# Kernel tuning notes

Hardware: AMD Instinct MI355X
Metric: run time of the kernel (lower is better)

## Reference

```python
import jax, jax.numpy as jnp
import numpy as np

D_MODEL = 1024
N_HEADS = 16
HEAD_D = D_MODEL // N_HEADS  # 64


def setup_inputs() -> dict:
    key = jax.random.key(0)
    ks = jax.random.split(key, 10)
    s = 1.0 / np.sqrt(D_MODEL)
    x = jax.random.normal(ks[0], (4, 2048, D_MODEL), dtype=jnp.float32)
    # Per-head Q/K/V linears stacked along a head axis: W [H, d_model, d], b [H, d]
    Wq = jax.random.uniform(ks[1], (N_HEADS, D_MODEL, HEAD_D), jnp.float32, -s, s)
    bq = jax.random.uniform(ks[2], (N_HEADS, HEAD_D), jnp.float32, -s, s)
    Wk = jax.random.uniform(ks[3], (N_HEADS, D_MODEL, HEAD_D), jnp.float32, -s, s)
    bk = jax.random.uniform(ks[4], (N_HEADS, HEAD_D), jnp.float32, -s, s)
    Wv = jax.random.uniform(ks[5], (N_HEADS, D_MODEL, HEAD_D), jnp.float32, -s, s)
    bv = jax.random.uniform(ks[6], (N_HEADS, HEAD_D), jnp.float32, -s, s)
    Wo = jax.random.uniform(ks[7], (D_MODEL, D_MODEL), jnp.float32, -s, s)
    bo = jax.random.uniform(ks[8], (D_MODEL,), jnp.float32, -s, s)
    return {"x": x, "Wq": Wq, "bq": bq, "Wk": Wk, "bk": bk,
            "Wv": Wv, "bv": bv, "Wo": Wo, "bo": bo}


def reference(x, Wq, bq, Wk, bk, Wv, bv, Wo, bo):
    # x: [B, S, M]; per-head projections -> [B, H, S, d]
    Q = jnp.einsum('bsm,hmd->bhsd', x, Wq) + bq[None, :, None, :]
    K = jnp.einsum('bsm,hmd->bhsd', x, Wk) + bk[None, :, None, :]
    V = jnp.einsum('bsm,hmd->bhsd', x, Wv) + bv[None, :, None, :]
    scale = 1.0 / jnp.sqrt(jnp.asarray(HEAD_D, dtype=x.dtype))
    scores = jnp.einsum('bhqd,bhkd->bhqk', Q, K) * scale  # [B, H, S, S]
    attn = jax.nn.softmax(scores, axis=-1)
    out = jnp.einsum('bhqk,bhkd->bhqd', attn, V)  # [B, H, S, d]
    B, H, S, d = out.shape
    out = out.transpose(0, 2, 1, 3).reshape(B, S, H * d)  # concat heads
    # final projection (dropout is identity in eval mode)
    return out @ Wo.T + bo
```

## Files before the change

kernel.cpp:

```cpp
#include <hip/hip_runtime.h>
#include <stdint.h>

#define DEVI __device__ __forceinline__

typedef float f32x4 __attribute__((ext_vector_type(4)));
typedef float f32x16 __attribute__((ext_vector_type(16)));
typedef float float4v __attribute__((ext_vector_type(4)));
typedef short short8 __attribute__((ext_vector_type(8)));
typedef uint16_t u16x4 __attribute__((ext_vector_type(4)));
typedef uint32_t u32x4 __attribute__((ext_vector_type(4)));
typedef int i32x2 __attribute__((ext_vector_type(2)));

static constexpr float QSCALE = 0.125f * 1.44269504088896340736f;

DEVI uint16_t f2bf(float f) {
  uint32_t u = __builtin_bit_cast(uint32_t, f);
  return (uint16_t)((u + 0x7FFFu + ((u >> 16) & 1u)) >> 16);
}

DEVI void gload_lds16(const void* g, void* lds) {
  __builtin_amdgcn_global_load_lds(
      reinterpret_cast<const uint32_t __attribute__((address_space(1)))*>(
          reinterpret_cast<uintptr_t>(g)),
      reinterpret_cast<uint32_t __attribute__((address_space(3)))*>(
          reinterpret_cast<uintptr_t>(lds)),
      16, 0, 0);
}

DEVI short8 lds_frag(const uint16_t* tile, int row, int kByte) {
  return *(const short8*)((const char*)tile + row * 128 + (kByte ^ ((row & 7) << 4)));
}

DEVI short8 frag256(const uint16_t* tile, int row, int j) {
  return *(const short8*)((const char*)tile + row * 256 + (((j ^ (row & 15)) << 4)));
}

DEVI f32x4 mfma16(short8 a, short8 b, f32x4 c) {
  return __builtin_amdgcn_mfma_f32_16x16x32_bf16(a, b, c, 0, 0, 0);
}
DEVI f32x16 mfma32(short8 a, short8 b, f32x16 c) {
  return __builtin_amdgcn_mfma_f32_32x32x16_bf16(a, b, c, 0, 0, 0);
}

DEVI uint32_t cvtpk(float lo, float hi) {
  uint32_t r;
  asm("v_cvt_pk_bf16_f32 %0, %1, %2" : "=v"(r) : "v"(lo), "v"(hi));
  return r;
}

DEVI void mk_pa(const f32x16& p0, const f32x16& p1, short8* pa) {
#pragma unroll
  for (int km = 0; km < 2; ++km) {
#pragma unroll
    for (int bb = 0; bb < 2; ++bb) {
      const f32x16& p = km ? p1 : p0;
      uint32_t X0 = cvtpk(p[8 * bb + 0], p[8 * bb + 1]);
      uint32_t Y0 = cvtpk(p[8 * bb + 4], p[8 * bb + 5]);
      uint32_t X1 = cvtpk(p[8 * bb + 2], p[8 * bb + 3]);
      uint32_t Y1 = cvtpk(p[8 * bb + 6], p[8 * bb + 7]);
      i32x2 s0 = __builtin_amdgcn_permlane32_swap((int)X0, (int)Y0, false, false);
      i32x2 s1 = __builtin_amdgcn_permlane32_swap((int)X1, (int)Y1, false, false);
      u32x4 dw = {(uint32_t)s0[0], (uint32_t)s1[0], (uint32_t)s0[1], (uint32_t)s1[1]};
      pa[km * 2 + bb] = __builtin_bit_cast(short8, dw);
    }
  }
}

DEVI float tree_sum(const f32x16& p0, const f32x16& p1) {
  float s[16];
#pragma unroll
  for (int r = 0; r < 16; ++r) s[r] = p0[r] + p1[r];
#pragma unroll
  for (int r = 0; r < 8; ++r) s[r] += s[r + 8];
#pragma unroll
  for (int r = 0; r < 4; ++r) s[r] += s[r + 4];
  return (s[0] + s[1]) + (s[2] + s[3]);
}

__global__ void k_prep(const float* __restrict__ x, const float* __restrict__ Wq,
                       const float* __restrict__ Wk, const float* __restrict__ Wv,
                       const float* __restrict__ Wo, uint16_t* __restrict__ xb,
                       uint16_t* __restrict__ Wt, uint16_t* __restrict__ Wob) {
  __shared__ float tile[64][65];
  const int bx = blockIdx.x, t = threadIdx.x;
  if (bx < 4608) {
    const float* src = (bx < 4096) ? x : Wo;
    uint16_t* dst = (bx < 4096) ? xb : Wob;
    const int i = (bx < 4096 ? bx : bx - 4096) * 256 + t;
    const float4v* p = (const float4v*)src + (size_t)i * 2;
    float4v a = p[0], b = p[1];
    alignas(16) uint16_t r[8];
    r[0] = f2bf(a[0]); r[1] = f2bf(a[1]); r[2] = f2bf(a[2]); r[3] = f2bf(a[3]);
    r[4] = f2bf(b[0]); r[5] = f2bf(b[1]); r[6] = f2bf(b[2]); r[7] = f2bf(b[3]);
    *((short8*)dst + i) = *(const short8*)r;
    return;
  }
  const int bq = bx - 4608;
  const int sect = bq >> 8, h = (bq >> 4) & 15, kc = bq & 15;
  const float* W = sect == 0 ? Wq : (sect == 1 ? Wk : Wv);
  const float scal = sect == 0 ? QSCALE : 1.0f;
  const int r = t >> 2, cbase = (t & 3) * 16;
  const float* src = W + ((size_t)(h * 1024 + kc * 64 + r)) * 64 + cbase;
#pragma unroll
  for (int j = 0; j < 4; ++j) {
    float4v v = *(const float4v*)(src + j * 4);
    tile[r][cbase + j * 4 + 0] = v[0];
    tile[r][cbase + j * 4 + 1] = v[1];
    tile[r][cbase + j * 4 + 2] = v[2];
    tile[r][cbase + j * 4 + 3] = v[3];
  }
  __syncthreads();
  const int dd = t >> 2, kp = (t & 3) * 16;
  alignas(16) uint16_t tmp[16];
#pragma unroll
  for (int j = 0; j < 16; ++j) tmp[j] = f2bf(tile[kp + j][dd] * scal);
  const int n = sect * 1024 + h * 64 + dd;
  uint16_t* dst = Wt + (size_t)n * 1024 + kc * 64 + kp;
  *(short8*)dst = *(const short8*)tmp;
  *((short8*)dst + 1) = *(const short8*)(tmp + 8);
}

template <int MODE>
__global__ __launch_bounds__(256, 2) void gemm_k1024(
    const uint16_t* __restrict__ A, const uint16_t* __restrict__ Bt, int tiles_n,
    const float* __restrict__ bias_q, const float* __restrict__ bias_k,
    const float* __restrict__ bias_v,
    uint16_t* __restrict__ Qws, uint16_t* __restrict__ Kws, uint16_t* __restrict__ Vtws,
    float* __restrict__ outf) {
  __shared__ uint16_t As[2][128 * 64];
  __shared__ uint16_t Bs[2][128 * 64];

  const int tid = threadIdx.x, lane = tid & 63, wv = tid >> 6;
  const int cpx = (MODE == 0) ? 192 : 64;
  const int bid = blockIdx.x;
  const int swz = (bid & 7) * cpx + (bid >> 3);
  const int m0 = (swz / tiles_n) * 128;
  const int n0 = (swz % tiles_n) * 128;
  const int wm = (wv >> 1) * 64, wn = (wv & 1) * 64;
  const int rin = lane >> 3;
  const int csw = ((lane & 7) ^ rin) * 16;

  const char* gA = (const char*)A;
  const char* gB = (const char*)Bt;

  f32x4 acc[4][4];
#pragma unroll
  for (int mi = 0; mi < 4; ++mi)
#pragma unroll
    for (int ni = 0; ni < 4; ++ni) acc[mi][ni] = (f32x4){0.f, 0.f, 0.f, 0.f};

  auto stage = [&](int buf, int kt) {
    const int k0b = kt * 128;
#pragma unroll
    for (int i = 0; i < 4; ++i) {
      const int rb = wv * 32 + i * 8;
      gload_lds16(gA + (size_t)(m0 + rb + rin) * 2048 + k0b + csw, &As[buf][rb * 64]);
      gload_lds16(gB + (size_t)(n0 + rb + rin) * 2048 + k0b + csw, &Bs[buf][rb * 64]);
    }
  };

  stage(0, 0);
  const int kb0 = (lane >> 4) * 16;
  for (int kt = 0; kt < 16; ++kt) {
    const int buf = kt & 1;
    __syncthreads();
    if (kt + 1 < 16) stage(buf ^ 1, kt + 1);
#pragma unroll
    for (int kk = 0; kk < 2; ++kk) {
      short8 af[4], bfr[4];
#pragma unroll
      for (int i = 0; i < 4; ++i) {
        af[i] = lds_frag(As[buf], wm + i * 16 + (lane & 15), kk * 64 + kb0);
        bfr[i] = lds_frag(Bs[buf], wn + i * 16 + (lane & 15), kk * 64 + kb0);
      }
#pragma unroll
      for (int mi = 0; mi < 4; ++mi)
#pragma unroll
        for (int ni = 0; ni < 4; ++ni) acc[mi][ni] = mfma16(af[mi], bfr[ni], acc[mi][ni]);
    }
    __syncthreads();
  }

  const int col0 = n0 + wn + (lane & 15);
  const int row0 = m0 + wm + ((lane >> 4) << 2);
  if (MODE == 1) {
#pragma unroll
    for (int ni = 0; ni < 4; ++ni) {
      const int n = col0 + ni * 16;
      const float bv = bias_q[n];
#pragma unroll
      for (int mi = 0; mi < 4; ++mi) {
        const int mrow = row0 + mi * 16;
#pragma unroll
        for (int r = 0; r < 4; ++r)
          outf[(size_t)(mrow + r) * 1024 + n] = acc[mi][ni][r] + bv;
      }
    }
  } else if (n0 >= 2048) {
    const int h = ((n0 + wn) >> 6) & 15;
    const int mbase = m0 + wm;
    const int b = mbase >> 11, sbase = mbase & 2047;
    const int bh = b * 16 + h;
    char* ep = (char*)&As[0][0] + wv * 8192;
#pragma unroll
    for (int ni = 0; ni < 4; ++ni) {
      const int dd = ni * 16 + (lane & 15);
      const float bv = bias_v[h * 64 + dd];
#pragma unroll
      for (int mi = 0; mi < 4; ++mi) {
#pragma unroll
        for (int r = 0; r < 4; ++r) {
          const int s = mi * 16 + ((lane >> 4) << 2) + r;
          *(uint16_t*)(ep + dd * 128 + ((s * 2) ^ ((dd & 7) << 4))) =
              f2bf(acc[mi][ni][r] + bv);
        }
      }
    }
#pragma unroll
    for (int it = 0; it < 8; ++it) {
      const int dd = it * 8 + (lane >> 3), c = lane & 7;
      short8 vv = *(const short8*)(ep + dd * 128 + ((c * 16) ^ ((dd & 7) << 4)));
      *(short8*)(Vtws + ((size_t)bh * 64 + dd) * 2048 + sbase + c * 8) = vv;
    }
  } else {
#pragma unroll
    for (int ni = 0; ni < 4; ++ni) {
      const int n = col0 + ni * 16;
      const int sect = n >> 10, h = (n >> 6) & 15, dd = n & 63;
      const float bv = (sect == 0) ? bias_q[h * 64 + dd] * QSCALE : bias_k[h * 64 + dd];
#pragma unroll
      for (int mi = 0; mi < 4; ++mi) {
        const int mrow = row0 + mi * 16;
        const int b = mrow >> 11, s = mrow & 2047;
        const int bh = b * 16 + h;
        uint16_t* dst = (sect == 0 ? Qws : Kws) + ((size_t)bh * 2048 + s) * 64 + dd;
#pragma unroll
        for (int r = 0; r < 4; ++r) dst[(size_t)r * 64] = f2bf(acc[mi][ni][r] + bv);
      }
    }
  }
}

__global__ __launch_bounds__(256, 2) void attn_fa(
    const uint16_t* __restrict__ Qws, const uint16_t* __restrict__ Kws,
    const uint16_t* __restrict__ Vtws, uint16_t* __restrict__ AttO) {
  __shared__ uint16_t SM[2][2][32 * 128];

  const int tid = threadIdx.x, lane = tid & 63, wq = tid >> 6;
  const int bid = blockIdx.x;
  const int bh = (bid & 7) * 8 + (bid >> 6);
  const int q0 = ((bid >> 3) & 7) * 256;
  const int hi = lane >> 5;
  const int qc = lane & 31;

  const uint16_t* Qb = Qws + (size_t)bh * (2048 * 64);
  const uint16_t* Kb = Kws + (size_t)bh * (2048 * 64);
  const uint16_t* Vb = Vtws + (size_t)bh * (64 * 2048);

  const int srow = lane >> 4;
  const int lchunk = lane & 15;

  short8 qf[2][4];
#pragma unroll
  for (int g = 0; g < 2; ++g)
#pragma unroll
    for (int c = 0; c < 4; ++c)
      qf[g][c] = *(const short8*)(Qb + (size_t)(q0 + wq * 64 + g * 32 + qc) * 64 +
                                  c * 16 + hi * 8);

  f32x16 oA0 = {}, oA1 = {}, oB0 = {}, oB1 = {};
  float lA = 0.0f, lB = 0.0f;

  auto stage = [&](int buf, int kt) {
    const int kv0 = kt * 64;
#pragma unroll
    for (int i = 0; i < 2; ++i) {
      const int rb = wq * 8 + i * 4;
      const int rt = rb + srow;
      const int j = lchunk ^ (rt & 15);
      const int jh = (j & 8) ? 32 : 0, jl = (j & 7) * 8;
      gload_lds16(Kb + (size_t)(kv0 + rt + jh) * 64 + jl,
                  (char*)&SM[buf][0][0] + rb * 256);
      gload_lds16(Vb + (size_t)(rt + jh) * 2048 + kv0 + jl,
                  (char*)&SM[buf][1][0] + rb * 256);
    }
  };

  stage(0, 0);
  for (int kt = 0; kt < 32; ++kt) {
    const int buf = kt & 1;
    __syncthreads();
    if (kt + 1 < 32) stage(buf ^ 1, kt + 1);
    const uint16_t* Kl = &SM[buf][0][0];
    const uint16_t* Vl = &SM[buf][1][0];

    f32x16 pA0 = {}, pA1 = {}, pB0 = {}, pB1 = {};
    __builtin_amdgcn_s_setprio(1);
#pragma unroll
    for (int c = 0; c < 4; ++c) {
      short8 k0 = frag256(Kl, qc, c * 2 + hi);
      short8 k1 = frag256(Kl, qc, 8 + c * 2 + hi);
      pA0 = mfma32(k0, qf[0][c], pA0);
      pA1 = mfma32(k1, qf[0][c], pA1);
      pB0 = mfma32(k0, qf[1][c], pB0);
      pB1 = mfma32(k1, qf[1][c], pB1);
    }
    __builtin_amdgcn_s_setprio(0);

    short8 paA[4], paB[4];
#pragma unroll
    for (int r = 0; r < 16; ++r) pA0[r] = __builtin_amdgcn_exp2f(pA0[r]);
#pragma unroll
    for (int r = 0; r < 16; ++r) pA1[r] = __builtin_amdgcn_exp2f(pA1[r]);
    lA += tree_sum(pA0, pA1);
    mk_pa(pA0, pA1, paA);
#pragma unroll
    for (int r = 0; r < 16; ++r) pB0[r] = __builtin_amdgcn_exp2f(pB0[r]);
#pragma unroll
    for (int r = 0; r < 16; ++r) pB1[r] = __builtin_amdgcn_exp2f(pB1[r]);
    lB += tree_sum(pB0, pB1);
    mk_pa(pB0, pB1, paB);

    __builtin_amdgcn_s_setprio(1);
#pragma unroll
    for (int ks = 0; ks < 4; ++ks) {
      short8 v0 = frag256(Vl, qc, ks * 2 + hi);
      short8 v1 = frag256(Vl, qc, 8 + ks * 2 + hi);
      oA0 = mfma32(v0, paA[ks], oA0);
      oA1 = mfma32(v1, paA[ks], oA1);
      oB0 = mfma32(v0, paB[ks], oB0);
      oB1 = mfma32(v1, paB[ks], oB1);
    }
    __builtin_amdgcn_s_setprio(0);
    __syncthreads();
  }
  lA += __shfl_xor(lA, 32, 64);
  lB += __shfl_xor(lB, 32, 64);

  const float invA = 1.0f / lA, invB = 1.0f / lB;
#pragma unroll
  for (int r = 0; r < 16; ++r) {
    oA0[r] *= invA; oA1[r] *= invA;
    oB0[r] *= invB; oB1[r] *= invB;
  }

  char* ep = (char*)&SM[0][0][0] + wq * 8192;
#pragma unroll
  for (int g = 0; g < 2; ++g)
#pragma unroll
    for (int no = 0; no < 2; ++no)
#pragma unroll
      for (int rg = 0; rg < 4; ++rg) {
        const f32x16& oo = g ? (no ? oB1 : oB0) : (no ? oA1 : oA0);
        const int row = g * 32 + qc;
        const int d0 = no * 32 + rg * 8 + hi * 4;
        u16x4 pk;
#pragma unroll
        for (int j = 0; j < 4; ++j) pk[j] = f2bf(oo[rg * 4 + j]);
        *(u16x4*)(ep + row * 128 + ((d0 * 2) ^ ((row & 7) << 4))) = pk;
      }
  const int b = bh >> 4, h = bh & 15;
#pragma unroll
  for (int it = 0; it < 8; ++it) {
    const int pos = it * 64 + lane;
    const int qq = pos >> 3, c = pos & 7;
    short8 vv = *(const short8*)(ep + qq * 128 + ((c * 16) ^ ((qq & 7) << 4)));
    *(short8*)(AttO + ((size_t)b * 2048 + q0 + wq * 64 + qq) * 1024 + h * 64 + c * 8) = vv;
  }
}


extern "C" void kernel_launch(void* const* d_in, const int* in_sizes, int n_in,
                              void* d_out, int out_size, void* d_ws, size_t ws_size,
                              hipStream_t stream) {
  (void)in_sizes; (void)n_in; (void)out_size; (void)ws_size;
  const float* x  = (const float*)d_in[0];
  const float* Wq = (const float*)d_in[1];
  const float* bq = (const float*)d_in[2];
  const float* Wk = (const float*)d_in[3];
  const float* bk = (const float*)d_in[4];
  const float* Wv = (const float*)d_in[5];
  const float* bv = (const float*)d_in[6];
  const float* Wo = (const float*)d_in[7];
  const float* bo = (const float*)d_in[8];
  float* out = (float*)d_out;

  char* ws = (char*)d_ws;
  uint16_t* Xb   = (uint16_t*)(ws);
  uint16_t* AttO = (uint16_t*)(ws);
  uint16_t* Wqkv = (uint16_t*)(ws + 16777216);
  uint16_t* Wob  = (uint16_t*)(ws + 23068672);
  uint16_t* Qws  = (uint16_t*)(ws + 25165824);
  uint16_t* Kws  = (uint16_t*)(ws + 41943040);
  uint16_t* Vt   = (uint16_t*)(ws + 58720256);

  k_prep<<<5376, 256, 0, stream>>>(x, Wq, Wk, Wv, Wo, Xb, Wqkv, Wob);
  gemm_k1024<0><<<64 * 24, 256, 0, stream>>>(Xb, Wqkv, 24, bq, bk, bv, Qws, Kws, Vt, nullptr);
  attn_fa<<<512, 256, 0, stream>>>(Qws, Kws, Vt, AttO);
  gemm_k1024<1><<<64 * 8, 256, 0, stream>>>(AttO, Wob, 8, bo, nullptr, nullptr,
                                            nullptr, nullptr, nullptr, out);
}
```

Before: 162.7 us.

## Prefetch two K-tiles ahead with explicit vmcnt waits in GEMM mainloop

The GEMM mainloop now issues global->LDS loads two stages ahead. Each iteration waits only for the older tile's loads via s_waitcnt vmcnt(8) instead of a full __syncthreads. All LDS fragments for both k-substeps are read into registers, followed by a barrier, before the buffer is refilled for tile kt+2. The MFMA block runs at raised wave priority, letting the next global loads overlap the matrix math. This costs extra fragment registers and relies on exact hand-counted outstanding-load numbers.

Measured after the change: 165.4 us. About the same (+1.6%).

```diff
diff --git a/kernel.cpp b/kernel.cpp
--- a/kernel.cpp
+++ b/kernel.cpp
@@ -160,25 +160,40 @@
   };
 
   stage(0, 0);
+  stage(1, 1);
   const int kb0 = (lane >> 4) * 16;
   for (int kt = 0; kt < 16; ++kt) {
     const int buf = kt & 1;
-    __syncthreads();
-    if (kt + 1 < 16) stage(buf ^ 1, kt + 1);
-#pragma unroll
-    for (int kk = 0; kk < 2; ++kk) {
-      short8 af[4], bfr[4];
+    if (kt < 15) asm volatile("s_waitcnt vmcnt(8)" ::: "memory");
+    else         asm volatile("s_waitcnt vmcnt(0)" ::: "memory");
+    __builtin_amdgcn_sched_barrier(0);
+    __builtin_amdgcn_s_barrier();
+    __builtin_amdgcn_sched_barrier(0);
+
+    short8 af[2][4], bfr[2][4];
+#pragma unroll
+    for (int kk = 0; kk < 2; ++kk)
 #pragma unroll
       for (int i = 0; i < 4; ++i) {
-        af[i] = lds_frag(As[buf], wm + i * 16 + (lane & 15), kk * 64 + kb0);
-        bfr[i] = lds_frag(Bs[buf], wn + i * 16 + (lane & 15), kk * 64 + kb0);
+        af[kk][i] = lds_frag(As[buf], wm + i * 16 + (lane & 15), kk * 64 + kb0);
+        bfr[kk][i] = lds_frag(Bs[buf], wn + i * 16 + (lane & 15), kk * 64 + kb0);
       }
+    asm volatile("s_waitcnt lgkmcnt(0)" ::: "memory");
+    __builtin_amdgcn_sched_barrier(0);
+    __builtin_amdgcn_s_barrier();
+    __builtin_amdgcn_sched_barrier(0);
+
+    if (kt + 2 < 16) stage(buf, kt + 2);
+
+    __builtin_amdgcn_s_setprio(1);
+#pragma unroll
+    for (int kk = 0; kk < 2; ++kk)
 #pragma unroll
       for (int mi = 0; mi < 4; ++mi)
 #pragma unroll
-        for (int ni = 0; ni < 4; ++ni) acc[mi][ni] = mfma16(af[mi], bfr[ni], acc[mi][ni]);
-    }
-    __syncthreads();
+        for (int ni = 0; ni < 4; ++ni)
+          acc[mi][ni] = mfma16(af[kk][mi], bfr[kk][ni], acc[mi][ni]);
+    __builtin_amdgcn_s_setprio(0);
   }
 
   const int col0 = n0 + wn + (lane & 15);
```
